# Kernel optimization log

Hardware: AMD Instinct MI355X
Metric: run time of the kernel (lower is better)

Reference implementation:

```python
import jax, jax.numpy as jnp
import numpy as np

D_MODEL = 1024
N_HEADS = 16
THRESHOLD = 0.8


def setup_inputs() -> dict:
    key = jax.random.key(0)
    ks = jax.random.split(key, 12)
    B, L, D = 2, 2048, D_MODEL
    s = 1.0 / np.sqrt(D)
    return {
        "q_x": jax.random.normal(ks[0], (B, L, D), jnp.float32),
        "k_x": jax.random.normal(ks[1], (B, L, D), jnp.float32),
        "v_x": jax.random.normal(ks[2], (B, L, D), jnp.float32),
        "energy": jax.random.normal(ks[3], (B, L, D), jnp.float32),
        "Wq": jax.random.normal(ks[4], (D, D), jnp.float32) * s,
        "bq": jnp.zeros((D,), jnp.float32),
        "Wk": jax.random.normal(ks[5], (D, D), jnp.float32) * s,
        "bk": jnp.zeros((D,), jnp.float32),
        "Wv": jax.random.normal(ks[6], (D, D), jnp.float32) * s,
        "bv": jnp.zeros((D,), jnp.float32),
        "Wo": jax.random.normal(ks[7], (D, D), jnp.float32) * s,
        "bo": jnp.zeros((D,), jnp.float32),
    }


def reference(q_x, k_x, v_x, energy, Wq, bq, Wk, bk, Wv, bv, Wo, bo):
    B, L, D = q_x.shape
    H = N_HEADS
    Dh = D // H
    # projections -> (B, H, L, Dh)
    Q = (q_x @ Wq + bq).reshape(B, L, H, Dh).transpose(0, 2, 1, 3)
    K = (k_x @ Wk + bk).reshape(B, -1, H, Dh).transpose(0, 2, 1, 3)
    V = (v_x @ Wv + bv).reshape(B, -1, H, Dh).transpose(0, 2, 1, 3)
    sc = jnp.einsum("bhqd,bhkd->bhqk", Q, K) / jnp.sqrt(jnp.float32(Dh))
    # energy mask: (B, Lk) -> broadcast over heads/queries
    mask = jnp.mean(jnp.abs(energy), axis=-1) > THRESHOLD  # (B, Lk)
    sc = jnp.where(mask[:, None, None, :], sc, -jnp.inf)
    w = jnp.nan_to_num(jax.nn.softmax(sc, axis=-1), nan=0.0)
    o = jnp.einsum("bhqk,bhkd->bhqd", w, V).transpose(0, 2, 1, 3).reshape(B, L, D)
    return o @ Wo + bo
```

## Files before the change

kernel.cpp:

```cpp
#include <hip/hip_runtime.h>
#include <hip/hip_bf16.h>
#include <cstdint>

#define DEVI static __device__ __forceinline__

typedef __attribute__((ext_vector_type(8))) short s16x8;
typedef __attribute__((ext_vector_type(4))) float f32x4;
typedef __attribute__((ext_vector_type(2))) unsigned int u32x2;

DEVI unsigned short f2bf(float f) {
  union { float f; unsigned int u; } v; v.f = f;
  return (unsigned short)((v.u + 0x7FFFu + ((v.u >> 16) & 1u)) >> 16);
}

DEVI unsigned int pk2bf(float a, float b) {
  __hip_bfloat162 h2 = __float22bfloat162_rn(float2{a, b});
  return *(unsigned int*)&h2;
}

DEVI void g2l16(const void* g, void* l) {
  __builtin_amdgcn_global_load_lds((const __attribute__((address_space(1))) void*)g,
                                   (__attribute__((address_space(3))) void*)l, 16, 0, 0);
}

__global__ __launch_bounds__(256) void prep_kernel(const float* __restrict__ a,
                                                   const float* __restrict__ b,
                                                   const float* __restrict__ c,
                                                   const float* __restrict__ energy,
                                                   unsigned short* __restrict__ oa,
                                                   unsigned short* __restrict__ ob,
                                                   unsigned short* __restrict__ oc,
                                                   int* __restrict__ flags,
                                                   const float* __restrict__ W0,
                                                   const float* __restrict__ W1,
                                                   const float* __restrict__ W2,
                                                   const float* __restrict__ W3,
                                                   unsigned short* __restrict__ T0,
                                                   unsigned short* __restrict__ T1,
                                                   unsigned short* __restrict__ T2,
                                                   unsigned short* __restrict__ T3) {
  const int gid = blockIdx.x;
  const int t = threadIdx.x;
  __shared__ float lds[64][65];
  if (gid < 6144) {
    const float* in = gid < 2048 ? a : gid < 4096 ? b : c;
    unsigned short* out = gid < 2048 ? oa : gid < 4096 ? ob : oc;
    const int blk = gid & 2047;
    int i = (blk * 256 + t) * 8;
    f32x4 x = *(const f32x4*)(in + i);
    f32x4 y = *(const f32x4*)(in + i + 4);
    s16x8 o;
    o[0] = (short)f2bf(x[0]); o[1] = (short)f2bf(x[1]);
    o[2] = (short)f2bf(x[2]); o[3] = (short)f2bf(x[3]);
    o[4] = (short)f2bf(y[0]); o[5] = (short)f2bf(y[1]);
    o[6] = (short)f2bf(y[2]); o[7] = (short)f2bf(y[3]);
    *(s16x8*)(out + i) = o;
    return;
  }
  if (gid < 10240) {
    const int row = gid - 6144;
    f32x4 v = *(const f32x4*)(energy + (size_t)row * 1024 + t * 4);
    float s = fabsf(v[0]) + fabsf(v[1]) + fabsf(v[2]) + fabsf(v[3]);
#pragma unroll
    for (int off = 1; off < 64; off <<= 1) s += __shfl_xor(s, off);
    if ((t & 63) == 0) lds[0][t >> 6] = s;
    __syncthreads();
    if (t == 0) {
      float tot = lds[0][0] + lds[0][1] + lds[0][2] + lds[0][3];
      flags[row] = (tot * (1.0f / 1024.0f) > 0.8f) ? 1 : 0;
    }
    return;
  }
  const int x = gid - 10240;
  const int z = x >> 8, rem = x & 255;
  const float* W = z == 0 ? W0 : z == 1 ? W1 : z == 2 ? W2 : W3;
  unsigned short* WT = z == 0 ? T0 : z == 1 ? T1 : z == 2 ? T2 : T3;
  const int n0 = (rem >> 4) * 64, k0 = (rem & 15) * 64;
#pragma unroll
  for (int p = 0; p < 4; p++) {
    int r = p * 16 + (t >> 4);
    int cc = (t & 15) * 4;
    f32x4 v = *(const f32x4*)(W + (size_t)(k0 + r) * 1024 + n0 + cc);
    lds[r][cc] = v[0]; lds[r][cc + 1] = v[1]; lds[r][cc + 2] = v[2]; lds[r][cc + 3] = v[3];
  }
  __syncthreads();
  const int cc = t >> 2, gk = t & 3;
#pragma unroll
  for (int hv = 0; hv < 2; hv++) {
    s16x8 o;
#pragma unroll
    for (int j = 0; j < 8; j++) o[j] = (short)f2bf(lds[gk * 16 + hv * 8 + j][cc]);
    *(s16x8*)(WT + (size_t)(n0 + cc) * 1024 + k0 + gk * 16 + hv * 8) = o;
  }
}

__global__ __launch_bounds__(256) void scan_kernel(const int* __restrict__ flags,
                                                   int* __restrict__ inv,
                                                   int* __restrict__ cnt) {
  const int b = blockIdx.x, t = threadIdx.x;
  const int* f = flags + b * 2048;
  int* iv = inv + b * 2048;
#pragma unroll
  for (int j = 0; j < 8; j++) iv[t * 8 + j] = 0;
  int loc[8], s = 0;
#pragma unroll
  for (int j = 0; j < 8; j++) { loc[j] = f[t * 8 + j]; s += loc[j]; }
  const int lane = t & 63, w = t >> 6;
  int ps = s;
#pragma unroll
  for (int off = 1; off < 64; off <<= 1) {
    int o = __shfl_up(ps, off);
    if (lane >= off) ps += o;
  }
  __shared__ int wsum[4];
  if (lane == 63) wsum[w] = ps;
  __syncthreads();
  int woff = 0;
  for (int i = 0; i < w; i++) woff += wsum[i];
  int excl = woff + ps - s;
#pragma unroll
  for (int j = 0; j < 8; j++) {
    if (loc[j]) { iv[excl] = t * 8 + j; excl++; }
  }
  if (t == 255) cnt[b] = woff + ps;
}

__global__ __launch_bounds__(256) void proj_qkv(const unsigned short* __restrict__ xq,
                                                const unsigned short* __restrict__ xk,
                                                const unsigned short* __restrict__ xv,
                                                const unsigned short* __restrict__ WTq,
                                                const unsigned short* __restrict__ WTk,
                                                const unsigned short* __restrict__ WTv,
                                                const float* __restrict__ bq,
                                                const float* __restrict__ bk,
                                                const float* __restrict__ bv,
                                                unsigned short* __restrict__ Qb,
                                                unsigned short* __restrict__ Kc,
                                                unsigned short* __restrict__ VTc,
                                                const int* __restrict__ inv,
                                                const int* __restrict__ cnt,
                                                float qsc) {
  const int z = blockIdx.z;
  const int m0 = blockIdx.x * 128;
  const int n0 = blockIdx.y * 64;
  const int b = m0 >> 11;
  const int lc0 = m0 & 2047;
  const int cb = (z == 0) ? 2048 : cnt[b];
  if (lc0 >= cb) return;

  const unsigned short* A  = z == 0 ? xq : z == 1 ? xk : xv;
  const unsigned short* BT = z == 0 ? WTq : z == 1 ? WTk : WTv;
  const float* bias        = z == 0 ? bq : z == 1 ? bk : bv;

  const int t = threadIdx.x;
  const int w = t >> 6, lane = t & 63;
  const int wr = w >> 1, wc = w & 1;
  const int lr = lane & 15, lg = lane >> 4;
  const int sr = lane >> 3, sg = lane & 7;

  int srow[4];
#pragma unroll
  for (int i = 0; i < 4; i++) {
    int r = (i * 4 + w) * 8 + sr;
    srow[i] = (z == 0) ? (m0 + r) : (b * 2048 + inv[b * 2048 + lc0 + r]);
  }

  __shared__ __align__(16) unsigned short As[128 * 64];
  __shared__ __align__(16) unsigned short Bs[64 * 64];

  f32x4 acc[4][2] = {};

  for (int kt = 0; kt < 1024; kt += 64) {
#pragma unroll
    for (int i = 0; i < 4; i++) {
      int r = (i * 4 + w) * 8 + sr;
      g2l16(A + (size_t)srow[i] * 1024 + kt + (sg ^ (r & 7)) * 8,
            (char*)As + (i * 4 + w) * 1024);
    }
#pragma unroll
    for (int i = 0; i < 2; i++) {
      int r = (i * 4 + w) * 8 + sr;
      g2l16(BT + (size_t)(n0 + r) * 1024 + kt + (sg ^ (r & 7)) * 8,
            (char*)Bs + (i * 4 + w) * 1024);
    }
    __syncthreads();
#pragma unroll
    for (int ks = 0; ks < 2; ks++) {
      s16x8 af[4], bf[2];
#pragma unroll
      for (int mi = 0; mi < 4; mi++) {
        int row = wr * 64 + mi * 16 + lr;
        af[mi] = *(const s16x8*)((const char*)As + row * 128 + (((ks * 4 + lg) ^ (row & 7)) * 16));
      }
#pragma unroll
      for (int nj = 0; nj < 2; nj++) {
        int row = wc * 32 + nj * 16 + lr;
        bf[nj] = *(const s16x8*)((const char*)Bs + row * 128 + (((ks * 4 + lg) ^ (row & 7)) * 16));
      }
#pragma unroll
      for (int mi = 0; mi < 4; mi++)
#pragma unroll
        for (int nj = 0; nj < 2; nj++)
          acc[mi][nj] = __builtin_amdgcn_mfma_f32_16x16x32_bf16(af[mi], bf[nj], acc[mi][nj], 0, 0, 0);
    }
    __syncthreads();
  }

  float bv2[2];
#pragma unroll
  for (int nj = 0; nj < 2; nj++) bv2[nj] = bias[n0 + wc * 32 + nj * 16 + lr];

#pragma unroll
  for (int mi = 0; mi < 4; mi++) {
    const int mloc = wr * 64 + mi * 16 + lg * 4;
#pragma unroll
    for (int nj = 0; nj < 2; nj++) {
      const int n = n0 + wc * 32 + nj * 16 + lr;
      if (z == 0) {
#pragma unroll
        for (int rg = 0; rg < 4; rg++)
          Qb[(size_t)(m0 + mloc + rg) * 1024 + n] = f2bf((acc[mi][nj][rg] + bv2[nj]) * qsc);
      } else if (z == 1) {
        const int h = n >> 6, dh = n & 63;
#pragma unroll
        for (int rg = 0; rg < 4; rg++) {
          int lc = lc0 + mloc + rg;
          if (lc < cb)
            Kc[((size_t)(b * 16 + h) * 2048 + lc) * 64 + dh] = f2bf(acc[mi][nj][rg] + bv2[nj]);
        }
      } else {
        const int h = n >> 6, dh = n & 63;
#pragma unroll
        for (int rg = 0; rg < 4; rg++) {
          int lc = lc0 + mloc + rg;
          if (lc < cb)
            VTc[((size_t)(b * 16 + h) * 64 + dh) * 2048 + lc] = f2bf(acc[mi][nj][rg] + bv2[nj]);
        }
      }
    }
  }
}

__global__ __launch_bounds__(256) void gemm_out(const unsigned short* __restrict__ A,
                                                const unsigned short* __restrict__ BT,
                                                const float* __restrict__ bias,
                                                float* __restrict__ out) {
  const int m0 = blockIdx.x * 128;
  const int n0 = blockIdx.y * 64;
  const int t = threadIdx.x;
  const int w = t >> 6, lane = t & 63;
  const int wr = w >> 1, wc = w & 1;
  const int lr = lane & 15, lg = lane >> 4;
  const int sr = lane >> 3, sg = lane & 7;

  __shared__ __align__(16) unsigned short As[128 * 64];
  __shared__ __align__(16) unsigned short Bs[64 * 64];

  f32x4 acc[4][2] = {};

  for (int kt = 0; kt < 1024; kt += 64) {
#pragma unroll
    for (int i = 0; i < 4; i++) {
      int r = (i * 4 + w) * 8 + sr;
      g2l16(A + (size_t)(m0 + r) * 1024 + kt + (sg ^ (r & 7)) * 8,
            (char*)As + (i * 4 + w) * 1024);
    }
#pragma unroll
    for (int i = 0; i < 2; i++) {
      int r = (i * 4 + w) * 8 + sr;
      g2l16(BT + (size_t)(n0 + r) * 1024 + kt + (sg ^ (r & 7)) * 8,
            (char*)Bs + (i * 4 + w) * 1024);
    }
    __syncthreads();
#pragma unroll
    for (int ks = 0; ks < 2; ks++) {
      s16x8 af[4], bf[2];
#pragma unroll
      for (int mi = 0; mi < 4; mi++) {
        int row = wr * 64 + mi * 16 + lr;
        af[mi] = *(const s16x8*)((const char*)As + row * 128 + (((ks * 4 + lg) ^ (row & 7)) * 16));
      }
#pragma unroll
      for (int nj = 0; nj < 2; nj++) {
        int row = wc * 32 + nj * 16 + lr;
        bf[nj] = *(const s16x8*)((const char*)Bs + row * 128 + (((ks * 4 + lg) ^ (row & 7)) * 16));
      }
#pragma unroll
      for (int mi = 0; mi < 4; mi++)
#pragma unroll
        for (int nj = 0; nj < 2; nj++)
          acc[mi][nj] = __builtin_amdgcn_mfma_f32_16x16x32_bf16(af[mi], bf[nj], acc[mi][nj], 0, 0, 0);
    }
    __syncthreads();
  }

  float bv2[2];
#pragma unroll
  for (int nj = 0; nj < 2; nj++) bv2[nj] = bias[n0 + wc * 32 + nj * 16 + lr];

#pragma unroll
  for (int mi = 0; mi < 4; mi++) {
    const int mb = m0 + wr * 64 + mi * 16 + lg * 4;
#pragma unroll
    for (int nj = 0; nj < 2; nj++) {
      const int n = n0 + wc * 32 + nj * 16 + lr;
#pragma unroll
      for (int rg = 0; rg < 4; rg++)
        out[(size_t)(mb + rg) * 1024 + n] = acc[mi][nj][rg] + bv2[nj];
    }
  }
}

__global__ __launch_bounds__(256) void attn_kernel(const unsigned short* __restrict__ Q,
                                                   const unsigned short* __restrict__ Kc,
                                                   const unsigned short* __restrict__ VTc,
                                                   const int* __restrict__ cnt,
                                                   unsigned short* __restrict__ O) {
  const int bh = blockIdx.x;
  const int qb = blockIdx.y;
  const int b = bh >> 4, h = bh & 15;
  const int t = threadIdx.x, w = t >> 6, lane = t & 63;
  const int lr = lane & 15, lg = lane >> 4;

  __shared__ __align__(16) unsigned short Ks[64 * 64];
  __shared__ __align__(16) unsigned short Vs[64 * 64];
  __shared__ __align__(16) unsigned short Ps[4][16 * 64];

  const size_t bh_off = (size_t)bh * 2048 * 64;
  const int q0 = qb * 64 + w * 16;
  const int cb = cnt[b];
  const int nkb = (cb + 63) >> 6;

  s16x8 qf[2];
#pragma unroll
  for (int ks = 0; ks < 2; ks++)
    qf[ks] = *(const s16x8*)(Q + ((size_t)(b * 2048 + q0 + lr)) * 1024 + h * 64 + ks * 32 + lg * 8);

  f32x4 oacc[4] = {};
  float lsum = 0.f;

  const int sr = lane >> 3, sg = lane & 7;
  for (int kb = 0; kb < nkb; kb++) {
#pragma unroll
    for (int i = 0; i < 2; i++) {
      int r = (i * 4 + w) * 8 + sr;
      g2l16(Kc + bh_off + (size_t)(kb * 64 + r) * 64 + (sg ^ (r & 7)) * 8,
            (char*)Ks + (i * 4 + w) * 1024);
    }
#pragma unroll
    for (int i = 0; i < 2; i++) {
      int r = (i * 4 + w) * 8 + sr;
      g2l16(VTc + bh_off + (size_t)r * 2048 + kb * 64 + (sg ^ (r & 7)) * 8,
            (char*)Vs + (i * 4 + w) * 1024);
    }
    __syncthreads();

    float p[4][4];
    __builtin_amdgcn_s_setprio(1);
#pragma unroll
    for (int t4 = 0; t4 < 4; t4++) {
      f32x4 s = {};
#pragma unroll
      for (int ks = 0; ks < 2; ks++) {
        int row = t4 * 16 + lr;
        s16x8 kf = *(const s16x8*)((const char*)Ks + row * 128 + (((ks * 4 + lg) ^ (row & 7)) * 16));
        s = __builtin_amdgcn_mfma_f32_16x16x32_bf16(kf, qf[ks], s, 0, 0, 0);
      }
      p[t4][0] = s[0]; p[t4][1] = s[1]; p[t4][2] = s[2]; p[t4][3] = s[3];
    }
    __builtin_amdgcn_s_setprio(0);

    if ((kb + 1) * 64 <= cb) {
#pragma unroll
      for (int t4 = 0; t4 < 4; t4++)
#pragma unroll
        for (int rg = 0; rg < 4; rg++) {
          float e = __builtin_amdgcn_exp2f(p[t4][rg]);
          p[t4][rg] = e;
          lsum += e;
        }
    } else {
      const int kbase = kb * 64 + lg * 4;
#pragma unroll
      for (int t4 = 0; t4 < 4; t4++)
#pragma unroll
        for (int rg = 0; rg < 4; rg++) {
          float e = __builtin_amdgcn_exp2f(p[t4][rg]);
          e = (kbase + t4 * 16 + rg < cb) ? e : 0.f;
          p[t4][rg] = e;
          lsum += e;
        }
    }

#pragma unroll
    for (int t4 = 0; t4 < 4; t4++) {
      u32x2 pw = {pk2bf(p[t4][0], p[t4][1]), pk2bf(p[t4][2], p[t4][3])};
      int byte = lr * 128 + ((t4 * 32 + lg * 8) ^ ((lr & 7) << 4));
      *(u32x2*)((char*)Ps + w * 2048 + byte) = pw;
    }

    __builtin_amdgcn_s_setprio(1);
#pragma unroll
    for (int ks = 0; ks < 2; ks++) {
      int byteA = lr * 128 + ((ks * 64 + lg * 16) ^ ((lr & 7) << 4));
      s16x8 af = *(const s16x8*)((const char*)Ps + w * 2048 + byteA);
#pragma unroll
      for (int dt = 0; dt < 4; dt++) {
        int row = dt * 16 + lr;
        s16x8 vf = *(const s16x8*)((const char*)Vs + row * 128 + (((ks * 4 + lg) ^ (row & 7)) * 16));
        oacc[dt] = __builtin_amdgcn_mfma_f32_16x16x32_bf16(af, vf, oacc[dt], 0, 0, 0);
      }
    }
    __builtin_amdgcn_s_setprio(0);
    __syncthreads();
  }

  lsum += __shfl_xor(lsum, 16);
  lsum += __shfl_xor(lsum, 32);

  float rinv[4];
#pragma unroll
  for (int rg = 0; rg < 4; rg++) {
    float ls = __shfl(lsum, lg * 4 + rg);
    rinv[rg] = (ls > 0.f) ? 1.0f / ls : 0.f;
  }
#pragma unroll
  for (int dt = 0; dt < 4; dt++)
#pragma unroll
    for (int rg = 0; rg < 4; rg++) {
      int q = q0 + lg * 4 + rg;
      int d = dt * 16 + lr;
      O[((size_t)(b * 2048 + q)) * 1024 + h * 64 + d] = f2bf(oacc[dt][rg] * rinv[rg]);
    }
}

extern "C" void kernel_launch(void* const* d_in, const int* in_sizes, int n_in,
                              void* d_out, int out_size, void* d_ws, size_t ws_size,
                              hipStream_t stream) {
  (void)in_sizes; (void)n_in; (void)out_size; (void)ws_size;
  const float* q_x = (const float*)d_in[0];
  const float* k_x = (const float*)d_in[1];
  const float* v_x = (const float*)d_in[2];
  const float* energy = (const float*)d_in[3];
  const float* Wq = (const float*)d_in[4];
  const float* bq = (const float*)d_in[5];
  const float* Wk = (const float*)d_in[6];
  const float* bk = (const float*)d_in[7];
  const float* Wv = (const float*)d_in[8];
  const float* bv = (const float*)d_in[9];
  const float* Wo = (const float*)d_in[10];
  const float* bo = (const float*)d_in[11];

  char* ws = (char*)d_ws;
  const size_t MB = 1024 * 1024;
  unsigned short* xq  = (unsigned short*)(ws + 0);
  unsigned short* xk  = (unsigned short*)(ws + 8 * MB);
  unsigned short* xv  = (unsigned short*)(ws + 16 * MB);
  unsigned short* WTq = (unsigned short*)(ws + 24 * MB);
  unsigned short* WTk = (unsigned short*)(ws + 26 * MB);
  unsigned short* WTv = (unsigned short*)(ws + 28 * MB);
  unsigned short* WTo = (unsigned short*)(ws + 30 * MB);
  unsigned short* Qb  = (unsigned short*)(ws + 32 * MB);
  unsigned short* Kc  = (unsigned short*)(ws + 40 * MB);
  unsigned short* VTc = (unsigned short*)(ws + 48 * MB);
  int* flags          = (int*)(ws + 56 * MB);
  int* inv            = (int*)(ws + 56 * MB + 16 * 1024);
  int* cnt            = (int*)(ws + 56 * MB + 32 * 1024);
  unsigned short* Ob  = xq;

  const float QSC = 0.18033688011112042f;

  prep_kernel<<<11264, 256, 0, stream>>>(q_x, k_x, v_x, energy, xq, xk, xv, flags,
                                         Wq, Wk, Wv, Wo, WTq, WTk, WTv, WTo);
  scan_kernel<<<2, 256, 0, stream>>>(flags, inv, cnt);

  proj_qkv<<<dim3(32, 16, 3), 256, 0, stream>>>(xq, xk, xv, WTq, WTk, WTv, bq, bk, bv,
                                                Qb, Kc, VTc, inv, cnt, QSC);

  attn_kernel<<<dim3(32, 32), 256, 0, stream>>>(Qb, Kc, VTc, cnt, Ob);

  gemm_out<<<dim3(32, 16), 256, 0, stream>>>(Ob, WTo, bo, (float*)d_out);
}
```

Baseline: 107.4 us.

## Double-buffer LDS tiles with 32-wide K steps in projection GEMMs

Both the QKV projection and output projection GEMMs now stage 32-wide K slices into two LDS buffers. The next slice's global-to-LDS loads are issued before computing on the current one, so memory latency overlaps with MFMA work. The XOR swizzle is adapted to 64-byte rows. In exchange there are twice as many K iterations and barriers, with the same total LDS footprint.

Result: slower. 116.5 us (+8.5%).

```diff
diff --git a/kernel.cpp b/kernel.cpp
--- a/kernel.cpp
+++ b/kernel.cpp
@@ -125,6 +125,7 @@
   if (t == 255) cnt[b] = woff + ps;
 }
 
+
 __global__ __launch_bounds__(256) void proj_qkv(const unsigned short* __restrict__ xq,
                                                 const unsigned short* __restrict__ xk,
                                                 const unsigned short* __restrict__ xv,
@@ -156,55 +157,67 @@
   const int w = t >> 6, lane = t & 63;
   const int wr = w >> 1, wc = w & 1;
   const int lr = lane & 15, lg = lane >> 4;
-  const int sr = lane >> 3, sg = lane & 7;
-
-  int srow[4];
-#pragma unroll
-  for (int i = 0; i < 4; i++) {
-    int r = (i * 4 + w) * 8 + sr;
-    srow[i] = (z == 0) ? (m0 + r) : (b * 2048 + inv[b * 2048 + lc0 + r]);
-  }
-
-  __shared__ __align__(16) unsigned short As[128 * 64];
-  __shared__ __align__(16) unsigned short Bs[64 * 64];
+
+  const int slr = lane >> 2;
+  const int sc = lane & 3;
+  int arow[2], akoff[2];
+#pragma unroll
+  for (int i = 0; i < 2; i++) {
+    int rt = (i * 4 + w) * 16 + slr;
+    arow[i] = (z == 0) ? (m0 + rt) : (b * 2048 + inv[b * 2048 + lc0 + rt]);
+    akoff[i] = 8 * (sc ^ ((rt >> 1) & 3));
+  }
+  const int brt = w * 16 + slr;
+  const int bkoff = 8 * (sc ^ ((brt >> 1) & 3));
+
+  __shared__ __align__(16) unsigned short As[2][128 * 32];
+  __shared__ __align__(16) unsigned short Bs[2][64 * 32];
 
   f32x4 acc[4][2] = {};
 
-  for (int kt = 0; kt < 1024; kt += 64) {
-#pragma unroll
-    for (int i = 0; i < 4; i++) {
-      int r = (i * 4 + w) * 8 + sr;
-      g2l16(A + (size_t)srow[i] * 1024 + kt + (sg ^ (r & 7)) * 8,
-            (char*)As + (i * 4 + w) * 1024);
-    }
-#pragma unroll
-    for (int i = 0; i < 2; i++) {
-      int r = (i * 4 + w) * 8 + sr;
-      g2l16(BT + (size_t)(n0 + r) * 1024 + kt + (sg ^ (r & 7)) * 8,
-            (char*)Bs + (i * 4 + w) * 1024);
-    }
+#define STAGE32(bb, kt)                                                          \
+  {                                                                              \
+    _Pragma("unroll")                                                            \
+    for (int i = 0; i < 2; i++)                                                  \
+      g2l16(A + (size_t)arow[i] * 1024 + (kt) + akoff[i],                        \
+            (char*)As[bb] + (i * 4 + w) * 1024);                                 \
+    g2l16(BT + (size_t)(n0 + brt) * 1024 + (kt) + bkoff,                         \
+          (char*)Bs[bb] + w * 1024);                                             \
+  }
+
+#define COMPUTE32(bb)                                                            \
+  {                                                                              \
+    s16x8 af[4], bf[2];                                                          \
+    _Pragma("unroll")                                                            \
+    for (int mi = 0; mi < 4; mi++) {                                             \
+      int row = wr * 64 + mi * 16 + lr;                                          \
+      af[mi] = *(const s16x8*)((const char*)As[bb] + row * 64 +                  \
+                               16 * (lg ^ ((row >> 1) & 3)));                    \
+    }                                                                            \
+    _Pragma("unroll")                                                            \
+    for (int nj = 0; nj < 2; nj++) {                                             \
+      int row = wc * 32 + nj * 16 + lr;                                          \
+      bf[nj] = *(const s16x8*)((const char*)Bs[bb] + row * 64 +                  \
+                               16 * (lg ^ ((row >> 1) & 3)));                    \
+    }                                                                            \
+    _Pragma("unroll")                                                            \
+    for (int mi = 0; mi < 4; mi++)                                               \
+      _Pragma("unroll")                                                          \
+      for (int nj = 0; nj < 2; nj++)                                             \
+        acc[mi][nj] = __builtin_amdgcn_mfma_f32_16x16x32_bf16(af[mi], bf[nj],    \
+                                                              acc[mi][nj], 0, 0, 0); \
+  }
+
+  STAGE32(0, 0);
+  __syncthreads();
+  int cur = 0;
+  for (int kt = 32; kt < 1024; kt += 32) {
+    STAGE32(cur ^ 1, kt);
+    COMPUTE32(cur);
     __syncthreads();
-#pragma unroll
-    for (int ks = 0; ks < 2; ks++) {
-      s16x8 af[4], bf[2];
-#pragma unroll
-      for (int mi = 0; mi < 4; mi++) {
-        int row = wr * 64 + mi * 16 + lr;
-        af[mi] = *(const s16x8*)((const char*)As + row * 128 + (((ks * 4 + lg) ^ (row & 7)) * 16));
-      }
-#pragma unroll
-      for (int nj = 0; nj < 2; nj++) {
-        int row = wc * 32 + nj * 16 + lr;
-        bf[nj] = *(const s16x8*)((const char*)Bs + row * 128 + (((ks * 4 + lg) ^ (row & 7)) * 16));
-      }
-#pragma unroll
-      for (int mi = 0; mi < 4; mi++)
-#pragma unroll
-        for (int nj = 0; nj < 2; nj++)
-          acc[mi][nj] = __builtin_amdgcn_mfma_f32_16x16x32_bf16(af[mi], bf[nj], acc[mi][nj], 0, 0, 0);
-    }
-    __syncthreads();
-  }
+    cur ^= 1;
+  }
+  COMPUTE32(cur);
 
   float bv2[2];
 #pragma unroll
@@ -239,6 +252,8 @@
       }
     }
   }
+#undef STAGE32
+#undef COMPUTE32
 }
 
 __global__ __launch_bounds__(256) void gemm_out(const unsigned short* __restrict__ A,
@@ -251,48 +266,66 @@
   const int w = t >> 6, lane = t & 63;
   const int wr = w >> 1, wc = w & 1;
   const int lr = lane & 15, lg = lane >> 4;
-  const int sr = lane >> 3, sg = lane & 7;
-
-  __shared__ __align__(16) unsigned short As[128 * 64];
-  __shared__ __align__(16) unsigned short Bs[64 * 64];
+  const int slr = lane >> 2, sc = lane & 3;
+
+  int arow[2], akoff[2];
+#pragma unroll
+  for (int i = 0; i < 2; i++) {
+    int rt = (i * 4 + w) * 16 + slr;
+    arow[i] = m0 + rt;
+    akoff[i] = 8 * (sc ^ ((rt >> 1) & 3));
+  }
+  const int brt = w * 16 + slr;
+  const int bkoff = 8 * (sc ^ ((brt >> 1) & 3));
+
+  __shared__ __align__(16) unsigned short As[2][128 * 32];
+  __shared__ __align__(16) unsigned short Bs[2][64 * 32];
 
   f32x4 acc[4][2] = {};
 
-  for (int kt = 0; kt < 1024; kt += 64) {
-#pragma unroll
-    for (int i = 0; i < 4; i++) {
-      int r = (i * 4 + w) * 8 + sr;
-      g2l16(A + (size_t)(m0 + r) * 1024 + kt + (sg ^ (r & 7)) * 8,
-            (char*)As + (i * 4 + w) * 1024);
-    }
-#pragma unroll
-    for (int i = 0; i < 2; i++) {
-      int r = (i * 4 + w) * 8 + sr;
-      g2l16(BT + (size_t)(n0 + r) * 1024 + kt + (sg ^ (r & 7)) * 8,
-            (char*)Bs + (i * 4 + w) * 1024);
-    }
+#define STAGE32(bb, kt)                                                          \
+  {                                                                              \
+    _Pragma("unroll")                                                            \
+    for (int i = 0; i < 2; i++)                                                  \
+      g2l16(A + (size_t)arow[i] * 1024 + (kt) + akoff[i],                        \
+            (char*)As[bb] + (i * 4 + w) * 1024);                                 \
+    g2l16(BT + (size_t)(n0 + brt) * 1024 + (kt) + bkoff,                         \
+          (char*)Bs[bb] + w * 1024);                                             \
+  }
+
+#define COMPUTE32(bb)                                                            \
+  {                                                                              \
+    s16x8 af[4], bf[2];                                                          \
+    _Pragma("unroll")                                                            \
+    for (int mi = 0; mi < 4; mi++) {                                             \
+      int row = wr * 64 + mi * 16 + lr;                                          \
+      af[mi] = *(const s16x8*)((const char*)As[bb] + row * 64 +                  \
+                               16 * (lg ^ ((row >> 1) & 3)));                    \
+    }                                                                            \
+    _Pragma("unroll")                                                            \
+    for (int nj = 0; nj < 2; nj++) {                                             \
+      int row = wc * 32 + nj * 16 + lr;                                          \
+      bf[nj] = *(const s16x8*)((const char*)Bs[bb] + row * 64 +                  \
+                               16 * (lg ^ ((row >> 1) & 3)));                    \
+    }                                                                            \
+    _Pragma("unroll")                                                            \
+    for (int mi = 0; mi < 4; mi++)                                               \
+      _Pragma("unroll")                                                          \
+      for (int nj = 0; nj < 2; nj++)                                             \
+        acc[mi][nj] = __builtin_amdgcn_mfma_f32_16x16x32_bf16(af[mi], bf[nj],    \
+                                                              acc[mi][nj], 0, 0, 0); \
+  }
+
+  STAGE32(0, 0);
+  __syncthreads();
+  int cur = 0;
+  for (int kt = 32; kt < 1024; kt += 32) {
+    STAGE32(cur ^ 1, kt);
+    COMPUTE32(cur);
     __syncthreads();
-#pragma unroll
-    for (int ks = 0; ks < 2; ks++) {
-      s16x8 af[4], bf[2];
-#pragma unroll
-      for (int mi = 0; mi < 4; mi++) {
-        int row = wr * 64 + mi * 16 + lr;
-        af[mi] = *(const s16x8*)((const char*)As + row * 128 + (((ks * 4 + lg) ^ (row & 7)) * 16));
-      }
-#pragma unroll
-      for (int nj = 0; nj < 2; nj++) {
-        int row = wc * 32 + nj * 16 + lr;
-        bf[nj] = *(const s16x8*)((const char*)Bs + row * 128 + (((ks * 4 + lg) ^ (row & 7)) * 16));
-      }
-#pragma unroll
-      for (int mi = 0; mi < 4; mi++)
-#pragma unroll
-        for (int nj = 0; nj < 2; nj++)
-          acc[mi][nj] = __builtin_amdgcn_mfma_f32_16x16x32_bf16(af[mi], bf[nj], acc[mi][nj], 0, 0, 0);
-    }
-    __syncthreads();
-  }
+    cur ^= 1;
+  }
+  COMPUTE32(cur);
 
   float bv2[2];
 #pragma unroll
@@ -309,6 +342,8 @@
         out[(size_t)(mb + rg) * 1024 + n] = acc[mi][nj][rg] + bv2[nj];
     }
   }
+#undef STAGE32
+#undef COMPUTE32
 }
 
 __global__ __launch_bounds__(256) void attn_kernel(const unsigned short* __restrict__ Q,
```
